# Optimization experiments

Measured on AMD Instinct MI355X. Metric: run time of the kernel, lower is better.

The kernel has to match this reference:

```python
import jax, jax.numpy as jnp
import numpy as np

N_NODES = 100000
N_EDGES = 1000000
IN_DIM = 37
HID = 64
BN_EPS = 1e-5


def setup_inputs() -> dict:
    key = jax.random.key(0)
    ks = jax.random.split(key, 12)
    return {
        "x": jax.random.normal(ks[0], (N_NODES, IN_DIM), dtype=jnp.float32),
        "edge_index": jax.random.randint(ks[1], (2, N_EDGES), 0, N_NODES, dtype=jnp.int64),
        "W1": jax.random.normal(ks[2], (IN_DIM, HID), dtype=jnp.float32) * 0.1,
        "W2": jax.random.normal(ks[3], (HID, HID), dtype=jnp.float32) * 0.1,
        "W3": jax.random.normal(ks[4], (HID, HID), dtype=jnp.float32) * 0.1,
        "b": jax.random.normal(ks[5], (3, HID), dtype=jnp.float32) * 0.1,
        "gamma": jax.random.uniform(ks[6], (3, HID), dtype=jnp.float32) + 0.5,
        "beta": jax.random.normal(ks[7], (3, HID), dtype=jnp.float32) * 0.1,
        "run_mean": jax.random.normal(ks[8], (3, HID), dtype=jnp.float32) * 0.1,
        "run_var": jax.random.uniform(ks[9], (3, HID), dtype=jnp.float32) + 0.5,
    }


def reference(x, edge_index, W1, W2, W3, b, gamma, beta, run_mean, run_var):
    N = x.shape[0]
    # GCN: add self loops, symmetric normalization D^{-1/2}(A+I)D^{-1/2}
    loops = jnp.arange(N, dtype=edge_index.dtype)
    row = jnp.concatenate([edge_index[0], loops])  # source
    col = jnp.concatenate([edge_index[1], loops])  # target (aggregation index)
    deg = jax.ops.segment_sum(jnp.ones_like(col, dtype=x.dtype), col, num_segments=N)
    dinv = jnp.where(deg > 0, jax.lax.rsqrt(deg), 0.0)
    enorm = (dinv[row] * dinv[col])[:, None]  # [E+N, 1]

    Ws = (W1, W2, W3)
    for i in range(3):
        h = x @ Ws[i]                                   # [N, HID]
        msg = enorm * h[row]                            # gather + scale
        h = jax.ops.segment_sum(msg, col, num_segments=N) + b[i]
        # BatchNorm1d (eval) + relu; dropout is identity at eval
        h = (h - run_mean[i]) * jax.lax.rsqrt(run_var[i] + BN_EPS) * gamma[i] + beta[i]
        h = jax.nn.relu(h)
        x = x + h if h.shape == x.shape else h          # residual when dims match
    return x
```

## Files before the change

### kernel.cpp

```cpp
#include <hip/hip_runtime.h>
#include <hip/hip_fp16.h>

#define NN 100000
#define NE 1000000
#define HID 64
#define BN_EPS 1e-5f

#define SCAN_EPB 1024
#define SCAN_NB ((NN + SCAN_EPB - 1) / SCAN_EPB)

typedef _Float16 hv2 __attribute__((ext_vector_type(2)));
typedef _Float16 hv8 __attribute__((ext_vector_type(8)));

static __device__ __forceinline__ float dot2acc(hv2 a, hv2 b, float c) {
#if __has_builtin(__builtin_amdgcn_fdot2)
    return __builtin_amdgcn_fdot2(a, b, c, false);
#else
    float r = c;
    asm("v_dot2_f32_f16 %0, %1, %2, %0" : "+v"(r) : "v"(a), "v"(b));
    return r;
#endif
}


__global__ void hist_rank_kernel(const int* __restrict__ col, int* __restrict__ deg,
                                 unsigned short* __restrict__ rank) {
    int e = blockIdx.x * 256 + threadIdx.x;
    if (e < NE) rank[e] = (unsigned short)atomicAdd(&deg[col[e]], 1);
}

__global__ __launch_bounds__(256) void scan_part(const int* __restrict__ deg,
                                                 int* __restrict__ partials) {
    __shared__ int sh[256];
    int t = threadIdx.x;
    int base = blockIdx.x * SCAN_EPB + t * 4;
    int s = 0;
    if (base + 3 < NN) {
        int4 v = *(const int4*)(deg + base);
        s = v.x + v.y + v.z + v.w;
    } else {
#pragma unroll
        for (int i = 0; i < 4; ++i) if (base + i < NN) s += deg[base + i];
    }
    sh[t] = s;
    __syncthreads();
    for (int d = 128; d > 0; d >>= 1) {
        if (t < d) sh[t] += sh[t + d];
        __syncthreads();
    }
    if (t == 0) partials[blockIdx.x] = sh[0];
}

__global__ __launch_bounds__(128) void scan_mid(const int* __restrict__ partials,
                                                int* __restrict__ poff) {
    __shared__ int sh[128];
    int t = threadIdx.x;
    int v = (t < SCAN_NB) ? partials[t] : 0;
    sh[t] = v;
    __syncthreads();
    for (int d = 1; d < 128; d <<= 1) {
        int u = (t >= d) ? sh[t - d] : 0;
        __syncthreads();
        sh[t] += u;
        __syncthreads();
    }
    if (t < SCAN_NB) poff[t] = sh[t] - v;
}

__global__ __launch_bounds__(256) void scan_fin(const int* __restrict__ deg,
                                                const int* __restrict__ poff,
                                                int* __restrict__ off,
                                                float* __restrict__ dinv) {
    __shared__ int sh[256];
    int t = threadIdx.x;
    int base = blockIdx.x * SCAN_EPB + t * 4;
    int v0 = 0, v1 = 0, v2 = 0, v3 = 0;
    if (base + 3 < NN) {
        int4 v = *(const int4*)(deg + base);
        v0 = v.x; v1 = v.y; v2 = v.z; v3 = v.w;
    } else {
        if (base + 0 < NN) v0 = deg[base + 0];
        if (base + 1 < NN) v1 = deg[base + 1];
        if (base + 2 < NN) v2 = deg[base + 2];
        if (base + 3 < NN) v3 = deg[base + 3];
    }
    int s = v0 + v1 + v2 + v3;
    sh[t] = s;
    __syncthreads();
    for (int d = 1; d < 256; d <<= 1) {
        int u = (t >= d) ? sh[t - d] : 0;
        __syncthreads();
        sh[t] += u;
        __syncthreads();
    }
    int run = poff[blockIdx.x] + sh[t] - s;
    if (base + 0 < NN) { off[base + 0] = run; run += v0; dinv[base + 0] = rsqrtf((float)(v0 + 1)); }
    if (base + 1 < NN) { off[base + 1] = run; run += v1; dinv[base + 1] = rsqrtf((float)(v1 + 1)); }
    if (base + 2 < NN) { off[base + 2] = run; run += v2; dinv[base + 2] = rsqrtf((float)(v2 + 1)); }
    if (base + 3 < NN) { off[base + 3] = run; run += v3; dinv[base + 3] = rsqrtf((float)(v3 + 1)); }
    if (blockIdx.x == 0 && t == 0) off[NN] = NE;
}

__global__ void fill_kernel(const int* __restrict__ row, const int* __restrict__ col,
                            const unsigned short* __restrict__ rank,
                            const int* __restrict__ off, int* __restrict__ csr) {
    int e = blockIdx.x * 256 + threadIdx.x;
    if (e >= NE) return;
    csr[off[col[e]] + (int)rank[e]] = row[e];
}

__global__ void pad_kernel(const float* __restrict__ x, const float* __restrict__ dinv,
                           _Float16* __restrict__ xp) {
    int i = blockIdx.x * 256 + threadIdx.x;
    if (i >= NN * 40) return;
    int n = i / 40, k = i - n * 40;
    float v = (k < 37) ? dinv[n] * x[n * 37 + k] : 0.f;
    xp[i] = (_Float16)v;
}

template <int NC, int KREAL, bool RES, bool W16, bool W32>
__global__ __launch_bounds__(256) void layer_kernel(
    const _Float16* __restrict__ xin, const float* __restrict__ dinv,
    const int* __restrict__ off, const int* __restrict__ csr,
    const float* __restrict__ W, const float* __restrict__ b,
    const float* __restrict__ gamma, const float* __restrict__ beta,
    const float* __restrict__ mean, const float* __restrict__ var,
    _Float16* __restrict__ out16, float* __restrict__ out32) {
    __shared__ _Float16 xs[4][8][NC * 8];
    const int tid  = threadIdx.x;
    const int w    = tid >> 6;
    const int l    = tid & 63;
    const int slot = l >> 3;
    const int c    = l & 7;
    const int nbase = (blockIdx.x * 4 + w) * 8;
    const hv8* __restrict__ x8 = (const hv8*)xin;

    hv2 wc[NC * 4];
#pragma unroll
    for (int q = 0; q < NC * 4; ++q) {
        float w0 = (2 * q     < KREAL) ? W[(2 * q)     * HID + l] : 0.f;
        float w1 = (2 * q + 1 < KREAL) ? W[(2 * q + 1) * HID + l] : 0.f;
        hv2 t = {(_Float16)w0, (_Float16)w1};
        wc[q] = t;
    }

    const int n = nbase + slot;
    if (c < NC) {
        hv8 accA = x8[(size_t)n * NC + c];
        hv8 accB = (hv8)(_Float16)0.f;
        int p  = off[n];
        int p1 = off[n + 1];
        for (; p + 3 < p1; p += 4) {
            int s0 = csr[p], s1 = csr[p + 1], s2 = csr[p + 2], s3 = csr[p + 3];
            hv8 v0 = x8[(size_t)s0 * NC + c];
            hv8 v1 = x8[(size_t)s1 * NC + c];
            hv8 v2 = x8[(size_t)s2 * NC + c];
            hv8 v3 = x8[(size_t)s3 * NC + c];
            accA += v0; accB += v1; accA += v2; accB += v3;
        }
        if (p + 1 < p1) {
            hv8 v0 = x8[(size_t)csr[p] * NC + c];
            hv8 v1 = x8[(size_t)csr[p + 1] * NC + c];
            accA += v0; accB += v1;
            p += 2;
        }
        if (p < p1) accA += x8[(size_t)csr[p] * NC + c];
        *(hv8*)&xs[w][slot][c * 8] = accA + accB;
    }
    __syncthreads();

    const float aa = gamma[l] * rsqrtf(var[l] + BN_EPS);
    const float cc = fmaf(b[l] - mean[l], aa, beta[l]);
    for (int i = 0; i < 8; ++i) {
        const int ni = nbase + i;
        float s = 0.f;
#pragma unroll
        for (int q0 = 0; q0 < NC; ++q0) {
            union { hv8 v; hv2 h[4]; } u;
            u.v = *(const hv8*)&xs[w][i][q0 * 8];
            s = dot2acc(u.h[0], wc[q0 * 4 + 0], s);
            s = dot2acc(u.h[1], wc[q0 * 4 + 1], s);
            s = dot2acc(u.h[2], wc[q0 * 4 + 2], s);
            s = dot2acc(u.h[3], wc[q0 * 4 + 3], s);
        }
        const float di = dinv[ni];
        float v = fmaf(s, di * aa, cc);
        v = fmaxf(v, 0.f);
        const size_t idx = (size_t)ni * HID + l;
        if (RES) v = fmaf((float)xin[(size_t)ni * (NC * 8) + l], 1.f / di, v);
        if (W32) out32[idx] = v;
        if (W16) out16[idx] = (_Float16)(v * di);
    }
}


static inline size_t align256(size_t x) { return (x + 255) & ~(size_t)255; }

extern "C" void kernel_launch(void* const* d_in, const int* in_sizes, int n_in,
                              void* d_out, int out_size, void* d_ws, size_t ws_size,
                              hipStream_t stream) {
    const float* x0   = (const float*)d_in[0];
    const int*   ei   = (const int*)d_in[1];
    const float* W1   = (const float*)d_in[2];
    const float* W2   = (const float*)d_in[3];
    const float* W3   = (const float*)d_in[4];
    const float* bb   = (const float*)d_in[5];
    const float* gam  = (const float*)d_in[6];
    const float* bet  = (const float*)d_in[7];
    const float* rmn  = (const float*)d_in[8];
    const float* rvr  = (const float*)d_in[9];
    float* out = (float*)d_out;

    char* w = (char*)d_ws;
    int*      deg      = (int*)w;      w += align256((size_t)NN * 4);
    int*      off      = (int*)w;      w += align256((size_t)(NN + 1) * 4);
    float*    dinv     = (float*)w;    w += align256((size_t)NN * 4);
    unsigned short* rank = (unsigned short*)w; w += align256((size_t)NE * 2);
    int*      partials = (int*)w;      w += align256((size_t)SCAN_NB * 4);
    int*      poff     = (int*)w;      w += align256((size_t)SCAN_NB * 4);
    int*      csr      = (int*)w;      w += align256((size_t)NE * 4);
    _Float16* xpad     = (_Float16*)w; w += align256((size_t)NN * 40 * 2);
    _Float16* hA16     = (_Float16*)w; w += align256((size_t)NN * HID * 2);
    _Float16* hB16     = (_Float16*)w; w += align256((size_t)NN * HID * 2);

    const int* row = ei;
    const int* col = ei + NE;

    dim3 blk(256);
    dim3 grE((NE + 255) / 256);
    dim3 grL(NN / 32);
    dim3 grPad((NN * 40 + 255) / 256);

    hipMemsetAsync(deg, 0, (size_t)NN * 4, stream);
    hist_rank_kernel<<<grE, blk, 0, stream>>>(col, deg, rank);
    scan_part<<<SCAN_NB, 256, 0, stream>>>(deg, partials);
    scan_mid<<<1, 128, 0, stream>>>(partials, poff);
    scan_fin<<<SCAN_NB, 256, 0, stream>>>(deg, poff, off, dinv);
    fill_kernel<<<grE, blk, 0, stream>>>(row, col, rank, off, csr);
    pad_kernel<<<grPad, blk, 0, stream>>>(x0, dinv, xpad);

    layer_kernel<5, 37, false, true, false><<<grL, blk, 0, stream>>>(
        xpad, dinv, off, csr, W1, bb + 0, gam + 0, bet + 0, rmn + 0, rvr + 0,
        hA16, nullptr);
    layer_kernel<8, 64, true, true, false><<<grL, blk, 0, stream>>>(
        hA16, dinv, off, csr, W2, bb + 64, gam + 64, bet + 64, rmn + 64, rvr + 64,
        hB16, nullptr);
    layer_kernel<8, 64, true, false, true><<<grL, blk, 0, stream>>>(
        hB16, dinv, off, csr, W3, bb + 128, gam + 128, bet + 128, rmn + 128, rvr + 128,
        nullptr, out);
}
```

Before: 259.0 us.

## Bucket nodes by degree so layer warps process similar-degree nodes together

Adds a degree histogram built in scan_fin and a bucket_fill kernel that writes a permutation of nodes sorted by in-degree bucket. The layer kernels then index nodes through this permutation, so the eight node slots in a wavefront have similar neighbor counts and lanes diverge less in the gather loop. It also folds the single-block scan_mid into scan_fin, with each block redoing the small prefix scan over the partials, which removes one launch. In exchange, output writes and self-feature reads become scattered through perm, adding an extra indirection and losing locality.

```diff
diff --git a/kernel.cpp b/kernel.cpp
--- a/kernel.cpp
+++ b/kernel.cpp
@@ -8,6 +8,7 @@
 
 #define SCAN_EPB 1024
 #define SCAN_NB ((NN + SCAN_EPB - 1) / SCAN_EPB)
+#define DBINS 64
 
 typedef _Float16 hv2 __attribute__((ext_vector_type(2)));
 typedef _Float16 hv8 __attribute__((ext_vector_type(8)));
@@ -51,28 +52,24 @@
     if (t == 0) partials[blockIdx.x] = sh[0];
 }
 
-__global__ __launch_bounds__(128) void scan_mid(const int* __restrict__ partials,
-                                                int* __restrict__ poff) {
-    __shared__ int sh[128];
+__global__ __launch_bounds__(256) void scan_fin(const int* __restrict__ deg,
+                                                const int* __restrict__ partials,
+                                                int* __restrict__ off,
+                                                float* __restrict__ dinv,
+                                                int* __restrict__ dbins) {
+    __shared__ int pv[128], ps[128], sh[256], hb[DBINS];
     int t = threadIdx.x;
-    int v = (t < SCAN_NB) ? partials[t] : 0;
-    sh[t] = v;
+    if (t < DBINS) hb[t] = 0;
+    if (t < 128) { int v = (t < SCAN_NB) ? partials[t] : 0; pv[t] = v; ps[t] = v; }
     __syncthreads();
     for (int d = 1; d < 128; d <<= 1) {
-        int u = (t >= d) ? sh[t - d] : 0;
-        __syncthreads();
-        sh[t] += u;
-        __syncthreads();
-    }
-    if (t < SCAN_NB) poff[t] = sh[t] - v;
-}
-
-__global__ __launch_bounds__(256) void scan_fin(const int* __restrict__ deg,
-                                                const int* __restrict__ poff,
-                                                int* __restrict__ off,
-                                                float* __restrict__ dinv) {
-    __shared__ int sh[256];
-    int t = threadIdx.x;
+        int u = (t >= d && t < 128) ? ps[t - d] : 0;
+        __syncthreads();
+        if (t < 128) ps[t] += u;
+        __syncthreads();
+    }
+    const int poffb = ps[blockIdx.x] - pv[blockIdx.x];
+
     int base = blockIdx.x * SCAN_EPB + t * 4;
     int v0 = 0, v1 = 0, v2 = 0, v3 = 0;
     if (base + 3 < NN) {
@@ -93,12 +90,39 @@
         sh[t] += u;
         __syncthreads();
     }
-    int run = poff[blockIdx.x] + sh[t] - s;
-    if (base + 0 < NN) { off[base + 0] = run; run += v0; dinv[base + 0] = rsqrtf((float)(v0 + 1)); }
-    if (base + 1 < NN) { off[base + 1] = run; run += v1; dinv[base + 1] = rsqrtf((float)(v1 + 1)); }
-    if (base + 2 < NN) { off[base + 2] = run; run += v2; dinv[base + 2] = rsqrtf((float)(v2 + 1)); }
-    if (base + 3 < NN) { off[base + 3] = run; run += v3; dinv[base + 3] = rsqrtf((float)(v3 + 1)); }
+    int run = poffb + sh[t] - s;
+    if (base + 0 < NN) { off[base + 0] = run; run += v0; dinv[base + 0] = rsqrtf((float)(v0 + 1)); atomicAdd(&hb[min(v0, DBINS - 1)], 1); }
+    if (base + 1 < NN) { off[base + 1] = run; run += v1; dinv[base + 1] = rsqrtf((float)(v1 + 1)); atomicAdd(&hb[min(v1, DBINS - 1)], 1); }
+    if (base + 2 < NN) { off[base + 2] = run; run += v2; dinv[base + 2] = rsqrtf((float)(v2 + 1)); atomicAdd(&hb[min(v2, DBINS - 1)], 1); }
+    if (base + 3 < NN) { off[base + 3] = run; run += v3; dinv[base + 3] = rsqrtf((float)(v3 + 1)); atomicAdd(&hb[min(v3, DBINS - 1)], 1); }
     if (blockIdx.x == 0 && t == 0) off[NN] = NE;
+    __syncthreads();
+    if (t < DBINS && hb[t]) atomicAdd(&dbins[t], hb[t]);
+}
+
+__global__ __launch_bounds__(256) void bucket_fill(const int* __restrict__ deg,
+                                                   const int* __restrict__ dbins,
+                                                   int* __restrict__ dcur,
+                                                   int* __restrict__ perm) {
+    __shared__ int dof[DBINS];
+    int t = threadIdx.x;
+    if (t < DBINS) {
+        int v = dbins[t];
+        int x = v;
+#pragma unroll
+        for (int d = 1; d < DBINS; d <<= 1) {
+            int u = __shfl_up(x, d);
+            if ((t & 63) >= d) x += u;
+        }
+        dof[t] = x - v;
+    }
+    __syncthreads();
+    int n = blockIdx.x * 256 + t;
+    if (n < NN) {
+        int k = min(deg[n], DBINS - 1);
+        int pos = dof[k] + atomicAdd(&dcur[k], 1);
+        perm[pos] = n;
+    }
 }
 
 __global__ void fill_kernel(const int* __restrict__ row, const int* __restrict__ col,
@@ -122,6 +146,7 @@
 __global__ __launch_bounds__(256) void layer_kernel(
     const _Float16* __restrict__ xin, const float* __restrict__ dinv,
     const int* __restrict__ off, const int* __restrict__ csr,
+    const int* __restrict__ perm,
     const float* __restrict__ W, const float* __restrict__ b,
     const float* __restrict__ gamma, const float* __restrict__ beta,
     const float* __restrict__ mean, const float* __restrict__ var,
@@ -144,7 +169,7 @@
         wc[q] = t;
     }
 
-    const int n = nbase + slot;
+    const int n = perm[nbase + slot];
     if (c < NC) {
         hv8 accA = x8[(size_t)n * NC + c];
         hv8 accB = (hv8)(_Float16)0.f;
@@ -172,7 +197,7 @@
     const float aa = gamma[l] * rsqrtf(var[l] + BN_EPS);
     const float cc = fmaf(b[l] - mean[l], aa, beta[l]);
     for (int i = 0; i < 8; ++i) {
-        const int ni = nbase + i;
+        const int ni = perm[nbase + i];
         float s = 0.f;
 #pragma unroll
         for (int q0 = 0; q0 < NC; ++q0) {
@@ -212,13 +237,15 @@
     float* out = (float*)d_out;
 
     char* w = (char*)d_ws;
-    int*      deg      = (int*)w;      w += align256((size_t)NN * 4);
+    int*      deg      = (int*)w;      w += align256((size_t)(NN + 2 * DBINS) * 4);
+    int*      dbins    = deg + NN;
+    int*      dcur     = deg + NN + DBINS;
     int*      off      = (int*)w;      w += align256((size_t)(NN + 1) * 4);
     float*    dinv     = (float*)w;    w += align256((size_t)NN * 4);
     unsigned short* rank = (unsigned short*)w; w += align256((size_t)NE * 2);
     int*      partials = (int*)w;      w += align256((size_t)SCAN_NB * 4);
-    int*      poff     = (int*)w;      w += align256((size_t)SCAN_NB * 4);
     int*      csr      = (int*)w;      w += align256((size_t)NE * 4);
+    int*      perm     = (int*)w;      w += align256((size_t)NN * 4);
     _Float16* xpad     = (_Float16*)w; w += align256((size_t)NN * 40 * 2);
     _Float16* hA16     = (_Float16*)w; w += align256((size_t)NN * HID * 2);
     _Float16* hB16     = (_Float16*)w; w += align256((size_t)NN * HID * 2);
@@ -228,24 +255,25 @@
 
     dim3 blk(256);
     dim3 grE((NE + 255) / 256);
+    dim3 grN((NN + 255) / 256);
     dim3 grL(NN / 32);
     dim3 grPad((NN * 40 + 255) / 256);
 
-    hipMemsetAsync(deg, 0, (size_t)NN * 4, stream);
+    hipMemsetAsync(deg, 0, (size_t)(NN + 2 * DBINS) * 4, stream);
     hist_rank_kernel<<<grE, blk, 0, stream>>>(col, deg, rank);
     scan_part<<<SCAN_NB, 256, 0, stream>>>(deg, partials);
-    scan_mid<<<1, 128, 0, stream>>>(partials, poff);
-    scan_fin<<<SCAN_NB, 256, 0, stream>>>(deg, poff, off, dinv);
+    scan_fin<<<SCAN_NB, 256, 0, stream>>>(deg, partials, off, dinv, dbins);
+    bucket_fill<<<grN, blk, 0, stream>>>(deg, dbins, dcur, perm);
     fill_kernel<<<grE, blk, 0, stream>>>(row, col, rank, off, csr);
     pad_kernel<<<grPad, blk, 0, stream>>>(x0, dinv, xpad);
 
     layer_kernel<5, 37, false, true, false><<<grL, blk, 0, stream>>>(
-        xpad, dinv, off, csr, W1, bb + 0, gam + 0, bet + 0, rmn + 0, rvr + 0,
+        xpad, dinv, off, csr, perm, W1, bb + 0, gam + 0, bet + 0, rmn + 0, rvr + 0,
         hA16, nullptr);
     layer_kernel<8, 64, true, true, false><<<grL, blk, 0, stream>>>(
-        hA16, dinv, off, csr, W2, bb + 64, gam + 64, bet + 64, rmn + 64, rvr + 64,
+        hA16, dinv, off, csr, perm, W2, bb + 64, gam + 64, bet + 64, rmn + 64, rvr + 64,
         hB16, nullptr);
     layer_kernel<8, 64, true, false, true><<<grL, blk, 0, stream>>>(
-        hB16, dinv, off, csr, W3, bb + 128, gam + 128, bet + 128, rmn + 128, rvr + 128,
+        hB16, dinv, off, csr, perm, W3, bb + 128, gam + 128, bet + 128, rmn + 128, rvr + 128,
         nullptr, out);
 }
```

New measurement: 583.5 us. 2.25x slower.
